# Performance work log

Measured on AMD Instinct MI355X. Metric: run time of the kernel, lower is better.

The kernel has to match this reference:

```python
import jax, jax.numpy as jnp
import numpy as np

N_E = 1024
E_DIM = 64
BETA = 0.25


def setup_inputs() -> dict:
    key = jax.random.key(0)
    k1, k2 = jax.random.split(key)
    z = jax.random.normal(k1, (32, 32, 32, E_DIM), dtype=jnp.float32)
    # torch init: uniform(-1/n_e, 1/n_e)
    codebook = jax.random.uniform(k2, (N_E, E_DIM), dtype=jnp.float32,
                                  minval=-1.0 / N_E, maxval=1.0 / N_E)
    return {"z": z, "codebook": codebook}


def reference(z, codebook):
    z_flat = z.reshape(-1, E_DIM)  # [N, e_dim]
    # squared euclidean distances: ||z||^2 + ||e||^2 - 2 z e^T
    d = (jnp.sum(z_flat ** 2, axis=1, keepdims=True)
         + jnp.sum(codebook ** 2, axis=1)
         - 2.0 * jnp.matmul(z_flat, codebook.T))  # [N, n_e]
    idx = jnp.argmin(d, axis=1)  # [N]
    z_q = codebook[idx].reshape(z.shape)
    sg = jax.lax.stop_gradient
    loss = jnp.mean((sg(z_q) - z) ** 2) + BETA * jnp.mean((z_q - sg(z)) ** 2)
    z_q_st = z + sg(z_q - z)  # straight-through estimator
    return z_q_st, idx, loss
```

## Files before the change

### kernel.cpp

```cpp
#include <hip/hip_runtime.h>

#define NROWS 32768
#define NE    1024
#define ED    64
#define CHUNK 128
#define NCH   (NE / CHUNK)
#define RPW   4
#define NW    8
#define RPB   (RPW * NW)

typedef float4 f4;
typedef float2 f2;

__global__ void vq_prep(const float* __restrict__ cb, float* __restrict__ ssq)
{
    int j = blockIdx.x * blockDim.x + threadIdx.x;
    const f4* crow = (const f4*)(cb + (size_t)j * ED);
    f4 v[16];
#pragma unroll
    for (int i = 0; i < 16; ++i) v[i] = crow[i];
    {
#pragma clang fp contract(off)
        float r0 = v[0].x*v[0].x, r1 = v[0].y*v[0].y;
        float r2 = v[0].z*v[0].z, r3 = v[0].w*v[0].w;
        float r4 = v[1].x*v[1].x, r5 = v[1].y*v[1].y;
        float r6 = v[1].z*v[1].z, r7 = v[1].w*v[1].w;
#pragma unroll
        for (int q = 2; q < 16; q += 2) {
            r0 += v[q].x*v[q].x;     r1 += v[q].y*v[q].y;
            r2 += v[q].z*v[q].z;     r3 += v[q].w*v[q].w;
            r4 += v[q+1].x*v[q+1].x; r5 += v[q+1].y*v[q+1].y;
            r6 += v[q+1].z*v[q+1].z; r7 += v[q+1].w*v[q+1].w;
        }
        ssq[j] = ((r0+r1)+(r2+r3)) + ((r4+r5)+(r6+r7));
    }
}

__global__ __launch_bounds__(512)
void vq_main(const float* __restrict__ z, const float* __restrict__ cb,
             const float* __restrict__ ssq, float* __restrict__ out,
             float* __restrict__ partials)
{
    __shared__ __align__(16) float et[ED * CHUNK];
    __shared__ int   idxsh[RPB];
    __shared__ float wsum[NW];

    const int tid  = threadIdx.x;
    const int lane = tid & 63;
    const int w    = tid >> 6;
    const int w_u  = __builtin_amdgcn_readfirstlane(w);
    const int rowbase = blockIdx.x * RPB;

    const float* zw = z + (size_t)(rowbase + w_u * RPW) * ED;

    float cn[RPW];
    {
        const int rl = (lane >> 3) & 3;
        const int jj = lane & 7;
        const float* zr = zw + (size_t)rl * ED;
        float a;
        {
#pragma clang fp contract(off)
            a = 0.f;
#pragma unroll
            for (int i = 0; i < 8; ++i) { float v = zr[8*i + jj]; a += v*v; }
        }
        a += __shfl_xor(a, 1);
        a += __shfl_xor(a, 2);
        a += __shfl_xor(a, 4);
#pragma unroll
        for (int r = 0; r < RPW; ++r) cn[r] = __shfl(a, r * 8);
    }

    float bestv[RPW];
    int   besti[RPW];
#pragma unroll
    for (int r = 0; r < RPW; ++r) { bestv[r] = INFINITY; besti[r] = 0; }

    const f2* et2 = (const f2*)et;

    for (int ch = 0; ch < NCH; ++ch) {
        __syncthreads();
        {
            const int c = tid & 127;
            const int h = tid >> 7;
            const f4* crow = (const f4*)(cb + (size_t)(ch * CHUNK + c) * ED
                                         + h * 16);
#pragma unroll
            for (int i = 0; i < 4; ++i) {
                f4 t = crow[i];
                const int dim = h * 16 + 4 * i;
                et[(dim+0) * CHUNK + c] = t.x;
                et[(dim+1) * CHUNK + c] = t.y;
                et[(dim+2) * CHUNK + c] = t.z;
                et[(dim+3) * CHUNK + c] = t.w;
            }
        }
        __syncthreads();

        f2 sv = ((const f2*)(ssq + ch * CHUNK))[lane];
        float svq[2] = {sv.x, sv.y};

        float acc[RPW][2];
#pragma unroll
        for (int r = 0; r < RPW; ++r) acc[r][0] = acc[r][1] = 0.f;

#pragma unroll 4
        for (int k4 = 0; k4 < 16; ++k4) {
            f2 e0 = et2[(4*k4+0) * 64 + lane];
            f2 e1 = et2[(4*k4+1) * 64 + lane];
            f2 e2 = et2[(4*k4+2) * 64 + lane];
            f2 e3 = et2[(4*k4+3) * 64 + lane];
            f4 z0 = *(const f4*)(zw + 0*ED + 4*k4);
            f4 z1 = *(const f4*)(zw + 1*ED + 4*k4);
            f4 z2 = *(const f4*)(zw + 2*ED + 4*k4);
            f4 z3 = *(const f4*)(zw + 3*ED + 4*k4);
#define ROWFMA(r, zz)                                                    \
            acc[r][0] = fmaf(zz.x, e0.x, acc[r][0]);                     \
            acc[r][1] = fmaf(zz.x, e0.y, acc[r][1]);                     \
            acc[r][0] = fmaf(zz.y, e1.x, acc[r][0]);                     \
            acc[r][1] = fmaf(zz.y, e1.y, acc[r][1]);                     \
            acc[r][0] = fmaf(zz.z, e2.x, acc[r][0]);                     \
            acc[r][1] = fmaf(zz.z, e2.y, acc[r][1]);                     \
            acc[r][0] = fmaf(zz.w, e3.x, acc[r][0]);                     \
            acc[r][1] = fmaf(zz.w, e3.y, acc[r][1]);
            ROWFMA(0, z0) ROWFMA(1, z1) ROWFMA(2, z2) ROWFMA(3, z3)
#undef ROWFMA
        }

        {
#pragma clang fp contract(off)
#pragma unroll
            for (int r = 0; r < RPW; ++r) {
#pragma unroll
                for (int q = 0; q < 2; ++q) {
                    float t1 = cn[r] + svq[q];
                    float d  = t1 - 2.0f * acc[r][q];
                    int j = ch * CHUNK + lane * 2 + q;
                    if (d < bestv[r]) { bestv[r] = d; besti[r] = j; }
                }
            }
        }
    }

    float lp = 0.f;
#pragma unroll
    for (int r = 0; r < RPW; ++r) {
        float v = bestv[r];
        int   i = besti[r];
#pragma unroll
        for (int m = 1; m < 64; m <<= 1) {
            float ov = __shfl_xor(v, m);
            int   oi = __shfl_xor(i, m);
            if (ov < v || (ov == v && oi < i)) { v = ov; i = oi; }
        }
        i &= (NE - 1);
        const int grow = rowbase + w * RPW + r;
        float zq, zz, diff, st;
        {
#pragma clang fp contract(off)
            zq   = cb[(size_t)i * ED + lane];
            zz   = z [(size_t)grow * ED + lane];
            diff = zq - zz;
            st   = zz + diff;
            lp  += diff * diff;
        }
        out[(size_t)grow * ED + lane] = st;
        if (lane == 0) idxsh[w * RPW + r] = i;
    }

#pragma unroll
    for (int m = 1; m < 64; m <<= 1) lp += __shfl_xor(lp, m);
    if (lane == 0) wsum[w] = lp;
    __syncthreads();

    if (tid < RPB) {
        int iv = idxsh[tid] & (NE - 1);
        out[(size_t)NROWS * ED + rowbase + tid] = (float)iv;
    }
    if (tid == 0)
        partials[blockIdx.x] = (((wsum[0]+wsum[1]) + (wsum[2]+wsum[3]))
                              + ((wsum[4]+wsum[5]) + (wsum[6]+wsum[7])));
}

__global__ void vq_finalize(const float* __restrict__ partials,
                            float* __restrict__ out)
{
    __shared__ float red[256];
    int t = threadIdx.x;
    float s = (partials[t] + partials[t + 256]) + (partials[t + 512] + partials[t + 768]);
    red[t] = s;
    __syncthreads();
    for (int m = 128; m > 0; m >>= 1) {
        if (t < m) red[t] += red[t + m];
        __syncthreads();
    }
    if (t == 0) {
        float mean = red[0] / (float)((size_t)NROWS * ED);
        out[(size_t)NROWS * ED + NROWS] = mean + 0.25f * mean;
    }
}

extern "C" void kernel_launch(void* const* d_in, const int* in_sizes, int n_in,
                              void* d_out, int out_size, void* d_ws, size_t ws_size,
                              hipStream_t stream)
{
    (void)in_sizes; (void)n_in; (void)out_size; (void)ws_size;
    const float* z  = (const float*)d_in[0];
    const float* cb = (const float*)d_in[1];
    float* out = (float*)d_out;
    float* ssq      = (float*)d_ws;
    float* partials = ssq + NE;

    vq_prep<<<4, 256, 0, stream>>>(cb, ssq);
    vq_main<<<1024, 512, 0, stream>>>(z, cb, ssq, out, partials);
    vq_finalize<<<1, 256, 0, stream>>>(partials, out);
}
```

Before: 84.70 us.

## Read pre-interleaved codebook from global memory instead of staging through LDS

```diff
diff --git a/kernel.cpp b/kernel.cpp
--- a/kernel.cpp
+++ b/kernel.cpp
@@ -3,16 +3,14 @@
 #define NROWS 32768
 #define NE    1024
 #define ED    64
-#define CHUNK 128
-#define NCH   (NE / CHUNK)
-#define RPW   4
-#define NW    8
+#define RPW   8
+#define NW    4
 #define RPB   (RPW * NW)
 
 typedef float4 f4;
-typedef float2 f2;
 
-__global__ void vq_prep(const float* __restrict__ cb, float* __restrict__ ssq)
+__global__ void vq_prep(const float* __restrict__ cb, f4* __restrict__ eTi,
+                        float* __restrict__ ssq)
 {
     int j = blockIdx.x * blockDim.x + threadIdx.x;
     const f4* crow = (const f4*)(cb + (size_t)j * ED);
@@ -34,14 +32,15 @@
         }
         ssq[j] = ((r0+r1)+(r2+r3)) + ((r4+r5)+(r6+r7));
     }
+#pragma unroll
+    for (int k4 = 0; k4 < 16; ++k4) eTi[(size_t)k4 * NE + j] = v[k4];
 }
 
-__global__ __launch_bounds__(512)
+__global__ __launch_bounds__(256)
 void vq_main(const float* __restrict__ z, const float* __restrict__ cb,
-             const float* __restrict__ ssq, float* __restrict__ out,
-             float* __restrict__ partials)
+             const f4* __restrict__ eTi, const float* __restrict__ ssq,
+             float* __restrict__ out, float* __restrict__ partials)
 {
-    __shared__ __align__(16) float et[ED * CHUNK];
     __shared__ int   idxsh[RPB];
     __shared__ float wsum[NW];
 
@@ -55,7 +54,7 @@
 
     float cn[RPW];
     {
-        const int rl = (lane >> 3) & 3;
+        const int rl = lane >> 3;
         const int jj = lane & 7;
         const float* zr = zw + (size_t)rl * ED;
         float a;
@@ -77,54 +76,32 @@
 #pragma unroll
     for (int r = 0; r < RPW; ++r) { bestv[r] = INFINITY; besti[r] = 0; }
 
-    const f2* et2 = (const f2*)et;
+    for (int g = 0; g < 16; ++g) {
+        const int c = g * 64 + lane;
+        const float sq = ssq[c];
 
-    for (int ch = 0; ch < NCH; ++ch) {
-        __syncthreads();
-        {
-            const int c = tid & 127;
-            const int h = tid >> 7;
-            const f4* crow = (const f4*)(cb + (size_t)(ch * CHUNK + c) * ED
-                                         + h * 16);
+        float acc[RPW];
 #pragma unroll
-            for (int i = 0; i < 4; ++i) {
-                f4 t = crow[i];
-                const int dim = h * 16 + 4 * i;
-                et[(dim+0) * CHUNK + c] = t.x;
-                et[(dim+1) * CHUNK + c] = t.y;
-                et[(dim+2) * CHUNK + c] = t.z;
-                et[(dim+3) * CHUNK + c] = t.w;
-            }
-        }
-        __syncthreads();
-
-        f2 sv = ((const f2*)(ssq + ch * CHUNK))[lane];
-        float svq[2] = {sv.x, sv.y};
-
-        float acc[RPW][2];
-#pragma unroll
-        for (int r = 0; r < RPW; ++r) acc[r][0] = acc[r][1] = 0.f;
+        for (int r = 0; r < RPW; ++r) acc[r] = 0.f;
 
 #pragma unroll 4
         for (int k4 = 0; k4 < 16; ++k4) {
-            f2 e0 = et2[(4*k4+0) * 64 + lane];
-            f2 e1 = et2[(4*k4+1) * 64 + lane];
-            f2 e2 = et2[(4*k4+2) * 64 + lane];
-            f2 e3 = et2[(4*k4+3) * 64 + lane];
+            f4 e  = eTi[(size_t)k4 * NE + c];
             f4 z0 = *(const f4*)(zw + 0*ED + 4*k4);
             f4 z1 = *(const f4*)(zw + 1*ED + 4*k4);
             f4 z2 = *(const f4*)(zw + 2*ED + 4*k4);
             f4 z3 = *(const f4*)(zw + 3*ED + 4*k4);
-#define ROWFMA(r, zz)                                                    \
-            acc[r][0] = fmaf(zz.x, e0.x, acc[r][0]);                     \
-            acc[r][1] = fmaf(zz.x, e0.y, acc[r][1]);                     \
-            acc[r][0] = fmaf(zz.y, e1.x, acc[r][0]);                     \
-            acc[r][1] = fmaf(zz.y, e1.y, acc[r][1]);                     \
-            acc[r][0] = fmaf(zz.z, e2.x, acc[r][0]);                     \
-            acc[r][1] = fmaf(zz.z, e2.y, acc[r][1]);                     \
-            acc[r][0] = fmaf(zz.w, e3.x, acc[r][0]);                     \
-            acc[r][1] = fmaf(zz.w, e3.y, acc[r][1]);
+            f4 z4 = *(const f4*)(zw + 4*ED + 4*k4);
+            f4 z5 = *(const f4*)(zw + 5*ED + 4*k4);
+            f4 z6 = *(const f4*)(zw + 6*ED + 4*k4);
+            f4 z7 = *(const f4*)(zw + 7*ED + 4*k4);
+#define ROWFMA(r, zz)                                 \
+            acc[r] = fmaf(e.x, zz.x, acc[r]);         \
+            acc[r] = fmaf(e.y, zz.y, acc[r]);         \
+            acc[r] = fmaf(e.z, zz.z, acc[r]);         \
+            acc[r] = fmaf(e.w, zz.w, acc[r]);
             ROWFMA(0, z0) ROWFMA(1, z1) ROWFMA(2, z2) ROWFMA(3, z3)
+            ROWFMA(4, z4) ROWFMA(5, z5) ROWFMA(6, z6) ROWFMA(7, z7)
 #undef ROWFMA
         }
 
@@ -132,13 +109,9 @@
 #pragma clang fp contract(off)
 #pragma unroll
             for (int r = 0; r < RPW; ++r) {
-#pragma unroll
-                for (int q = 0; q < 2; ++q) {
-                    float t1 = cn[r] + svq[q];
-                    float d  = t1 - 2.0f * acc[r][q];
-                    int j = ch * CHUNK + lane * 2 + q;
-                    if (d < bestv[r]) { bestv[r] = d; besti[r] = j; }
-                }
+                float t1 = cn[r] + sq;
+                float d  = t1 - 2.0f * acc[r];
+                if (d < bestv[r]) { bestv[r] = d; besti[r] = c; }
             }
         }
     }
@@ -179,8 +152,7 @@
         out[(size_t)NROWS * ED + rowbase + tid] = (float)iv;
     }
     if (tid == 0)
-        partials[blockIdx.x] = (((wsum[0]+wsum[1]) + (wsum[2]+wsum[3]))
-                              + ((wsum[4]+wsum[5]) + (wsum[6]+wsum[7])));
+        partials[blockIdx.x] = (wsum[0] + wsum[1]) + (wsum[2] + wsum[3]);
 }
 
 __global__ void vq_finalize(const float* __restrict__ partials,
@@ -209,10 +181,12 @@
     const float* z  = (const float*)d_in[0];
     const float* cb = (const float*)d_in[1];
     float* out = (float*)d_out;
-    float* ssq      = (float*)d_ws;
+
+    f4*    eTi      = (f4*)d_ws;
+    float* ssq      = (float*)(eTi + 16 * NE);
     float* partials = ssq + NE;
 
-    vq_prep<<<4, 256, 0, stream>>>(cb, ssq);
-    vq_main<<<1024, 512, 0, stream>>>(z, cb, ssq, out, partials);
+    vq_prep<<<4, 256, 0, stream>>>(cb, eTi, ssq);
+    vq_main<<<1024, 256, 0, stream>>>(z, cb, eTi, ssq, out, partials);
     vq_finalize<<<1, 256, 0, stream>>>(partials, out);
 }
```

New measurement: 124.8 us. 1.47x slower.
